# Performance work log

Hardware: AMD Instinct MI355X
Metric: run time of the kernel (lower is better)

## Reference

```python
import jax, jax.numpy as jnp
import numpy as np

N = 50000          # nodes
E = 1_600_000      # edges (avg degree 32)
F_IN = 512         # input feature dim
H = 256            # hidden_channels
C = 121            # num_classes (PPI)
L = 4              # num_layers
ALPHA = 0.5
THETA = 1.0


def setup_inputs() -> dict:
    key = jax.random.key(0)
    ks = jax.random.split(key, 8)
    x = jax.random.normal(ks[0], (N, F_IN), jnp.float32)
    edge_src = jax.random.randint(ks[1], (E,), 0, N, jnp.int32)
    edge_dst = jax.random.randint(ks[2], (E,), 0, N, jnp.int32)
    edge_weight = jax.random.uniform(ks[3], (E,), jnp.float32)
    s0 = 1.0 / np.sqrt(F_IN).astype(np.float32)
    lin0_w = jax.random.uniform(ks[4], (F_IN, H), jnp.float32, -s0, s0)
    lin0_b = jnp.zeros((H,), jnp.float32)
    conv_ws = jax.random.normal(ks[5], (L, H, H), jnp.float32) / np.float32(np.sqrt(H))
    s1 = 1.0 / np.sqrt(H).astype(np.float32)
    lin1_w = jax.random.uniform(ks[6], (H, C), jnp.float32, -s1, s1)
    lin1_b = jnp.zeros((C,), jnp.float32)
    return {
        "x": x, "edge_src": edge_src, "edge_dst": edge_dst,
        "edge_weight": edge_weight, "lin0_w": lin0_w, "lin0_b": lin0_b,
        "conv_ws": conv_ws, "lin1_w": lin1_w, "lin1_b": lin1_b,
    }


def reference(x, edge_src, edge_dst, edge_weight, lin0_w, lin0_b, conv_ws, lin1_w, lin1_b):
    # input projection + relu (dropout p=0 -> identity)
    x = jax.nn.relu(x @ lin0_w + lin0_b)          # [N, H]
    x0 = x
    for layer in range(L):
        beta = np.float32(np.log(THETA / (layer + 1) + 1.0))
        # sparse propagation: h = A @ x  (edge-wise gather * weight, scatter-add)
        msg = x[edge_src] * edge_weight[:, None]   # [E, H]
        h = jax.ops.segment_sum(msg, edge_dst, num_segments=N)  # [N, H]
        # GCN2Conv (shared_weights=True, normalize=False)
        h = (1.0 - ALPHA) * h + ALPHA * x0
        h = (1.0 - beta) * h + beta * (h @ conv_ws[layer])
        # residual + relu
        x = jax.nn.relu(h + x)
    return x @ lin1_w + lin1_b                    # [N, C]
```

## Files before the change

### kernel.cpp

```cpp
#include <hip/hip_runtime.h>
#include <math.h>

#define N_NODES 50000
#define E_EDGES 1600000
#define F_INDIM 512
#define H_DIM   256
#define C_OUT   121
#define L_LAYERS 4

typedef unsigned short u16;
typedef short bf16x8 __attribute__((ext_vector_type(8)));
typedef float f32x4  __attribute__((ext_vector_type(4)));

__device__ __forceinline__ float bf2f(u16 h) {
    return __uint_as_float(((unsigned int)h) << 16);
}
__device__ __forceinline__ u16 f2bf(float f) {
    unsigned int u = __float_as_uint(f);
    unsigned int r = u + 0x7FFFu + ((u >> 16) & 1u);
    return (u16)(r >> 16);
}

__global__ void prep_kernel(const float* __restrict__ l0w, const float* __restrict__ cw,
                            const float* __restrict__ l1w, u16* __restrict__ WT0,
                            u16* __restrict__ WTc, u16* __restrict__ WT1,
                            int* __restrict__ cnt) {
    int i = blockIdx.x * blockDim.x + threadIdx.x;
    if (i < 131072) {
        int n = i >> 9, k = i & 511;
        WT0[i] = f2bf(l0w[(long)k * H_DIM + n]);
        return;
    }
    i -= 131072;
    if (i < 262144) {
        int l = i >> 16, j = i & 65535, n = j >> 8, k = j & 255;
        WTc[(l << 16) + j] = f2bf(cw[(long)l * 65536 + (long)k * H_DIM + n]);
        return;
    }
    i -= 262144;
    if (i < 32768) {
        int n = i >> 8, k = i & 255;
        WT1[i] = (n < C_OUT) ? f2bf(l1w[(long)k * C_OUT + n]) : (u16)0;
        return;
    }
    i -= 32768;
    if (i < N_NODES) cnt[i] = 0;
}

__global__ void hist_kernel(const int* __restrict__ dst, int* __restrict__ deg) {
    int i = blockIdx.x * blockDim.x + threadIdx.x;
    if (i < E_EDGES / 4) {
        int4 d4 = reinterpret_cast<const int4*>(dst)[i];
        if (d4.x >= 0 && d4.x < N_NODES) atomicAdd(&deg[d4.x], 1);
        if (d4.y >= 0 && d4.y < N_NODES) atomicAdd(&deg[d4.y], 1);
        if (d4.z >= 0 && d4.z < N_NODES) atomicAdd(&deg[d4.z], 1);
        if (d4.w >= 0 && d4.w < N_NODES) atomicAdd(&deg[d4.w], 1);
    }
}

__global__ void scan_kernel(int* cnt, int* __restrict__ row_ptr) {
    __shared__ int sums[1024];
    const int t = threadIdx.x;
    const int CH = (N_NODES + 1023) / 1024;
    const int base = t * CH;
    int s = 0;
    for (int i = 0; i < CH; ++i) {
        int idx = base + i;
        if (idx < N_NODES) s += cnt[idx];
    }
    sums[t] = s;
    __syncthreads();
    for (int off = 1; off < 1024; off <<= 1) {
        int v = (t >= off) ? sums[t - off] : 0;
        __syncthreads();
        sums[t] += v;
        __syncthreads();
    }
    int run = (t == 0) ? 0 : sums[t - 1];
    for (int i = 0; i < CH; ++i) {
        int idx = base + i;
        if (idx < N_NODES) {
            int dv = cnt[idx];
            row_ptr[idx] = run;
            cnt[idx] = run;
            run += dv;
        }
    }
    if (t == 1023) row_ptr[N_NODES] = run;
}

__global__ void scatter_kernel(const int* __restrict__ src, const int* __restrict__ dst,
                               const float* __restrict__ w,
                               int* __restrict__ cnt, int* __restrict__ s_src,
                               float* __restrict__ s_w) {
    int i = blockIdx.x * blockDim.x + threadIdx.x;
    if (i < E_EDGES / 4) {
        int4   s4 = reinterpret_cast<const int4*>(src)[i];
        int4   d4 = reinterpret_cast<const int4*>(dst)[i];
        float4 w4 = reinterpret_cast<const float4*>(w)[i];
        int   sv[4] = {s4.x, s4.y, s4.z, s4.w};
        int   dv[4] = {d4.x, d4.y, d4.z, d4.w};
        float wv[4] = {w4.x, w4.y, w4.z, w4.w};
        #pragma unroll
        for (int u = 0; u < 4; ++u) {
            int d = dv[u];
            if (d < 0) d = 0; if (d >= N_NODES) d = N_NODES - 1;
            long idx = atomicAdd(&cnt[d], 1);
            if (idx < 0) idx = 0; if (idx >= E_EDGES) idx = E_EDGES - 1;
            s_src[idx] = sv[u];
            s_w[idx]   = wv[u];
        }
    }
}

template <int LAST>
__global__ __launch_bounds__(512) void layer_kernel(
        const int* __restrict__ row_ptr, const int* __restrict__ s_src,
        const float* __restrict__ s_w, const u16* __restrict__ Xin,
        const u16* __restrict__ X0, u16* __restrict__ Xout,
        const u16* __restrict__ WT, float beta,
        const u16* __restrict__ WT1, const float* __restrict__ l1b,
        float* __restrict__ outp) {
    __shared__ __align__(16) u16 hs[16 * H_DIM];
    const int w  = threadIdx.x >> 6;
    const int l  = threadIdx.x & 63;
    const int hi = l >> 4, lo = l & 15;
    const int half = l >> 5;
    const int q    = l & 31;
    const int bm = blockIdx.x * 16;

    for (int i = 0; i < 2; ++i) {
        const int rl  = w * 2 + i;
        const int row = bm + rl;
        int beg = row_ptr[row], end = row_ptr[row + 1];
        if (beg < 0) beg = 0; if (end > E_EDGES) end = E_EDGES;
        float accA[8] = {}, accB[8] = {};
        for (int e = beg; e < end; e += 4) {
            const int eA = e + half;
            const int eB = e + 2 + half;
            const int cA = (eA < end) ? eA : end - 1;
            const int cB = (eB < end) ? eB : end - 1;
            float wA = (eA < end) ? s_w[cA] : 0.f;
            float wB = (eB < end) ? s_w[cB] : 0.f;
            int sA = s_src[cA]; if (sA < 0) sA = 0; if (sA >= N_NODES) sA = N_NODES - 1;
            int sB = s_src[cB]; if (sB < 0) sB = 0; if (sB >= N_NODES) sB = N_NODES - 1;
            bf16x8 vA = *reinterpret_cast<const bf16x8*>(Xin + (long)sA * H_DIM + q * 8);
            bf16x8 vB = *reinterpret_cast<const bf16x8*>(Xin + (long)sB * H_DIM + q * 8);
            #pragma unroll
            for (int j = 0; j < 8; ++j) {
                accA[j] += wA * bf2f((u16)vA[j]);
                accB[j] += wB * bf2f((u16)vB[j]);
            }
        }
        float acc[8];
        #pragma unroll
        for (int j = 0; j < 8; ++j) {
            float s = accA[j] + accB[j];
            s += __shfl_xor(s, 32);
            acc[j] = s;
        }
        if (l < 32) {
            bf16x8 x0 = *reinterpret_cast<const bf16x8*>(X0 + (long)row * H_DIM + q * 8);
            bf16x8 ov;
            #pragma unroll
            for (int j = 0; j < 8; ++j)
                ov[j] = (short)f2bf(0.5f * acc[j] + 0.5f * bf2f((u16)x0[j]));
            const int off = rl * 512 + ((q * 16) ^ ((rl & 7) << 4));
            *reinterpret_cast<bf16x8*>((char*)hs + off) = ov;
        }
    }
    __syncthreads();

    const int col0 = w * 32;
    f32x4 acc[2];
    acc[0] = (f32x4){0.f, 0.f, 0.f, 0.f};
    acc[1] = (f32x4){0.f, 0.f, 0.f, 0.f};

    for (int k0 = 0; k0 < H_DIM; k0 += 32) {
        const int aoff = lo * 512 + (((k0 * 2) + hi * 16) ^ ((lo & 7) << 4));
        bf16x8 a = *reinterpret_cast<const bf16x8*>((const char*)hs + aoff);
        #pragma unroll
        for (int t = 0; t < 2; ++t) {
            bf16x8 b = *reinterpret_cast<const bf16x8*>(
                    WT + (long)(col0 + t * 16 + lo) * H_DIM + k0 + hi * 8);
            acc[t] = __builtin_amdgcn_mfma_f32_16x16x32_bf16(a, b, acc[t], 0, 0, 0);
        }
    }

    if (LAST) __syncthreads();

    #pragma unroll
    for (int t = 0; t < 2; ++t) {
        const int col = col0 + t * 16 + lo;
        #pragma unroll
        for (int r = 0; r < 4; ++r) {
            const int rl  = hi * 4 + r;
            const int row = bm + rl;
            const int hoff = rl * 512 + ((col * 2) ^ ((rl & 7) << 4));
            float hv = bf2f(*reinterpret_cast<const u16*>((const char*)hs + hoff));
            long idx = (long)row * H_DIM + col;
            float v = (1.f - beta) * hv + beta * acc[t][r] + bf2f(Xin[idx]);
            u16 vb = f2bf(fmaxf(v, 0.f));
            if (!LAST) {
                Xout[idx] = vb;
            } else {
                *reinterpret_cast<u16*>((char*)hs + hoff) = vb;
            }
        }
    }

    if (LAST) {
        __syncthreads();
        const int c1 = w * 16;
        f32x4 acc2 = (f32x4){0.f, 0.f, 0.f, 0.f};
        for (int k0 = 0; k0 < H_DIM; k0 += 32) {
            const int aoff = lo * 512 + (((k0 * 2) + hi * 16) ^ ((lo & 7) << 4));
            bf16x8 a = *reinterpret_cast<const bf16x8*>((const char*)hs + aoff);
            bf16x8 b = *reinterpret_cast<const bf16x8*>(
                    WT1 + (long)(c1 + lo) * H_DIM + k0 + hi * 8);
            acc2 = __builtin_amdgcn_mfma_f32_16x16x32_bf16(a, b, acc2, 0, 0, 0);
        }
        const int col = c1 + lo;
        if (col < C_OUT) {
            const float bias = l1b[col];
            #pragma unroll
            for (int r = 0; r < 4; ++r) {
                const int row = bm + hi * 4 + r;
                outp[(long)row * C_OUT + col] = acc2[r] + bias;
            }
        }
    }
}

template <int K, int NT>
__global__ __launch_bounds__(256) void mfma_gemm_kernel(
        const float* __restrict__ Aptr, const u16* __restrict__ WT,
        const float* __restrict__ bias,
        u16* __restrict__ X, u16* __restrict__ X0) {
    const int w  = threadIdx.x >> 6;
    const int l  = threadIdx.x & 63;
    const int hi = l >> 4, lo = l & 15;
    const int bm = blockIdx.x * 16;
    const int col0 = w * (NT * 16);

    f32x4 acc[NT];
    #pragma unroll
    for (int t = 0; t < NT; ++t) acc[t] = (f32x4){0.f, 0.f, 0.f, 0.f};

    for (int k0 = 0; k0 < K; k0 += 32) {
        bf16x8 a;
        const float* ap = Aptr + (long)(bm + lo) * K + k0 + hi * 8;
        float4 f0 = *reinterpret_cast<const float4*>(ap);
        float4 f1 = *reinterpret_cast<const float4*>(ap + 4);
        a[0] = (short)f2bf(f0.x); a[1] = (short)f2bf(f0.y);
        a[2] = (short)f2bf(f0.z); a[3] = (short)f2bf(f0.w);
        a[4] = (short)f2bf(f1.x); a[5] = (short)f2bf(f1.y);
        a[6] = (short)f2bf(f1.z); a[7] = (short)f2bf(f1.w);
        #pragma unroll
        for (int t = 0; t < NT; ++t) {
            bf16x8 b = *reinterpret_cast<const bf16x8*>(
                    WT + (long)(col0 + t * 16 + lo) * K + k0 + hi * 8);
            acc[t] = __builtin_amdgcn_mfma_f32_16x16x32_bf16(a, b, acc[t], 0, 0, 0);
        }
    }

    #pragma unroll
    for (int t = 0; t < NT; ++t) {
        const int col = col0 + t * 16 + lo;
        #pragma unroll
        for (int r = 0; r < 4; ++r) {
            const int row = bm + hi * 4 + r;
            float v = fmaxf(acc[t][r] + bias[col], 0.f);
            u16 h = f2bf(v);
            long idx = (long)row * H_DIM + col;
            X[idx] = h; X0[idx] = h;
        }
    }
}

extern "C" void kernel_launch(void* const* d_in, const int* in_sizes, int n_in,
                              void* d_out, int out_size, void* d_ws, size_t ws_size,
                              hipStream_t stream) {
    const float* x_in = (const float*)d_in[0];
    const int*   esrc = (const int*)d_in[1];
    const int*   edst = (const int*)d_in[2];
    const float* ew   = (const float*)d_in[3];
    const float* l0w  = (const float*)d_in[4];
    const float* l0b  = (const float*)d_in[5];
    const float* cw   = (const float*)d_in[6];
    const float* l1w  = (const float*)d_in[7];
    const float* l1b  = (const float*)d_in[8];
    float* out = (float*)d_out;
    (void)in_sizes; (void)n_in; (void)out_size;

    char* ws = (char*)d_ws;
    auto al = [](size_t x) { return (x + 255) & ~(size_t)255; };
    size_t o = 0;
    const size_t NHb = (size_t)N_NODES * H_DIM * sizeof(u16);
    u16* Xa = (u16*)(ws + o);  o += al(NHb);
    u16* Xb = (u16*)(ws + o);  o += al(NHb);
    u16* X0 = (u16*)(ws + o);  o += al(NHb);
    int* row_ptr = (int*)(ws + o); o += al((N_NODES + 1) * sizeof(int));
    int* cnt     = (int*)(ws + o); o += al((size_t)N_NODES * sizeof(int));
    int* s_src   = (int*)(ws + o); o += al((size_t)E_EDGES * sizeof(int));
    float* s_w   = (float*)(ws + o); o += al((size_t)E_EDGES * sizeof(float));
    u16* WT0 = (u16*)(ws + o); o += al((size_t)H_DIM * F_INDIM * sizeof(u16));
    u16* WTc = (u16*)(ws + o); o += al((size_t)L_LAYERS * H_DIM * H_DIM * sizeof(u16));
    u16* WT1 = (u16*)(ws + o); o += al((size_t)128 * H_DIM * sizeof(u16));
    if (ws_size < o) return;

    const int MBLK = N_NODES / 16;

    prep_kernel<<<1860, 256, 0, stream>>>(l0w, cw, l1w, WT0, WTc, WT1, cnt);

    mfma_gemm_kernel<F_INDIM, 4><<<MBLK, 256, 0, stream>>>(x_in, WT0, l0b, Xa, X0);

    hist_kernel<<<(E_EDGES / 4 + 255) / 256, 256, 0, stream>>>(edst, cnt);
    scan_kernel<<<1, 1024, 0, stream>>>(cnt, row_ptr);
    scatter_kernel<<<(E_EDGES / 4 + 255) / 256, 256, 0, stream>>>(esrc, edst, ew,
                                                                  cnt, s_src, s_w);

    u16* Xcur = Xa;
    u16* Xnxt = Xb;
    for (int l = 0; l < L_LAYERS - 1; ++l) {
        float beta = logf(1.0f / (float)(l + 1) + 1.0f);
        layer_kernel<0><<<MBLK, 512, 0, stream>>>(
            row_ptr, s_src, s_w, Xcur, X0, Xnxt,
            WTc + (size_t)l * H_DIM * H_DIM, beta,
            nullptr, nullptr, nullptr);
        u16* tmp = Xcur; Xcur = Xnxt; Xnxt = tmp;
    }
    {
        const int l = L_LAYERS - 1;
        float beta = logf(1.0f / (float)(l + 1) + 1.0f);
        layer_kernel<1><<<MBLK, 512, 0, stream>>>(
            row_ptr, s_src, s_w, Xcur, X0, nullptr,
            WTc + (size_t)l * H_DIM * H_DIM, beta,
            WT1, l1b, out);
    }
}
```

Baseline: 1.096 ms.

## Stage block edge lists in LDS and retile input projection GEMM

```diff
diff --git a/kernel.cpp b/kernel.cpp
--- a/kernel.cpp
+++ b/kernel.cpp
@@ -7,6 +7,7 @@
 #define H_DIM   256
 #define C_OUT   121
 #define L_LAYERS 4
+#define MCAP    1280
 
 typedef unsigned short u16;
 typedef short bf16x8 __attribute__((ext_vector_type(8)));
@@ -122,12 +123,25 @@
         const u16* __restrict__ WT1, const float* __restrict__ l1b,
         float* __restrict__ outp) {
     __shared__ __align__(16) u16 hs[16 * H_DIM];
+    __shared__ int   ms_src[MCAP];
+    __shared__ float ms_w[MCAP];
     const int w  = threadIdx.x >> 6;
     const int l  = threadIdx.x & 63;
     const int hi = l >> 4, lo = l & 15;
     const int half = l >> 5;
     const int q    = l & 31;
     const int bm = blockIdx.x * 16;
+
+    const int mbeg = row_ptr[bm];
+    int mspan = row_ptr[bm + 16] - mbeg;
+    if (mspan < 0) mspan = 0;
+    const int mlim = (mspan < MCAP) ? mspan : MCAP;
+    for (int j = threadIdx.x; j < mlim; j += 512) {
+        long gj = (long)mbeg + j;
+        if (gj >= 0 && gj < E_EDGES) { ms_src[j] = s_src[gj]; ms_w[j] = s_w[gj]; }
+        else                         { ms_src[j] = 0;         ms_w[j] = 0.f; }
+    }
+    __syncthreads();
 
     for (int i = 0; i < 2; ++i) {
         const int rl  = w * 2 + i;
@@ -140,10 +154,18 @@
             const int eB = e + 2 + half;
             const int cA = (eA < end) ? eA : end - 1;
             const int cB = (eB < end) ? eB : end - 1;
-            float wA = (eA < end) ? s_w[cA] : 0.f;
-            float wB = (eB < end) ? s_w[cB] : 0.f;
-            int sA = s_src[cA]; if (sA < 0) sA = 0; if (sA >= N_NODES) sA = N_NODES - 1;
-            int sB = s_src[cB]; if (sB < 0) sB = 0; if (sB >= N_NODES) sB = N_NODES - 1;
+            const int rA = cA - mbeg;
+            const int rB = cB - mbeg;
+            int sA; float wA;
+            int sB; float wB;
+            if (rA >= 0 && rA < MCAP) { sA = ms_src[rA]; wA = ms_w[rA]; }
+            else                      { sA = s_src[cA];  wA = s_w[cA]; }
+            if (rB >= 0 && rB < MCAP) { sB = ms_src[rB]; wB = ms_w[rB]; }
+            else                      { sB = s_src[cB];  wB = s_w[cB]; }
+            if (eA >= end) wA = 0.f;
+            if (eB >= end) wB = 0.f;
+            if (sA < 0) sA = 0; if (sA >= N_NODES) sA = N_NODES - 1;
+            if (sB < 0) sB = 0; if (sB >= N_NODES) sB = N_NODES - 1;
             bf16x8 vA = *reinterpret_cast<const bf16x8*>(Xin + (long)sA * H_DIM + q * 8);
             bf16x8 vB = *reinterpret_cast<const bf16x8*>(Xin + (long)sB * H_DIM + q * 8);
             #pragma unroll
@@ -232,50 +254,64 @@
     }
 }
 
-template <int K, int NT>
-__global__ __launch_bounds__(256) void mfma_gemm_kernel(
+__global__ __launch_bounds__(512) void lin0_kernel(
         const float* __restrict__ Aptr, const u16* __restrict__ WT,
         const float* __restrict__ bias,
         u16* __restrict__ X, u16* __restrict__ X0) {
     const int w  = threadIdx.x >> 6;
     const int l  = threadIdx.x & 63;
     const int hi = l >> 4, lo = l & 15;
-    const int bm = blockIdx.x * 16;
-    const int col0 = w * (NT * 16);
-
-    f32x4 acc[NT];
+    const int bm = blockIdx.x * 32;
+    const int col0 = w * 32;
+
+    f32x4 acc[2][2];
     #pragma unroll
-    for (int t = 0; t < NT; ++t) acc[t] = (f32x4){0.f, 0.f, 0.f, 0.f};
-
-    for (int k0 = 0; k0 < K; k0 += 32) {
-        bf16x8 a;
-        const float* ap = Aptr + (long)(bm + lo) * K + k0 + hi * 8;
-        float4 f0 = *reinterpret_cast<const float4*>(ap);
-        float4 f1 = *reinterpret_cast<const float4*>(ap + 4);
-        a[0] = (short)f2bf(f0.x); a[1] = (short)f2bf(f0.y);
-        a[2] = (short)f2bf(f0.z); a[3] = (short)f2bf(f0.w);
-        a[4] = (short)f2bf(f1.x); a[5] = (short)f2bf(f1.y);
-        a[6] = (short)f2bf(f1.z); a[7] = (short)f2bf(f1.w);
-        #pragma unroll
-        for (int t = 0; t < NT; ++t) {
+    for (int h = 0; h < 2; ++h)
+        #pragma unroll
+        for (int t = 0; t < 2; ++t) acc[h][t] = (f32x4){0.f, 0.f, 0.f, 0.f};
+
+    for (int k0 = 0; k0 < F_INDIM; k0 += 32) {
+        bf16x8 a[2];
+        #pragma unroll
+        for (int h = 0; h < 2; ++h) {
+            const int grow = bm + h * 16 + lo;
+            bf16x8 av = {0, 0, 0, 0, 0, 0, 0, 0};
+            if (grow < N_NODES) {
+                const float* ap = Aptr + (long)grow * F_INDIM + k0 + hi * 8;
+                float4 f0 = *reinterpret_cast<const float4*>(ap);
+                float4 f1 = *reinterpret_cast<const float4*>(ap + 4);
+                av[0] = (short)f2bf(f0.x); av[1] = (short)f2bf(f0.y);
+                av[2] = (short)f2bf(f0.z); av[3] = (short)f2bf(f0.w);
+                av[4] = (short)f2bf(f1.x); av[5] = (short)f2bf(f1.y);
+                av[6] = (short)f2bf(f1.z); av[7] = (short)f2bf(f1.w);
+            }
+            a[h] = av;
+        }
+        #pragma unroll
+        for (int t = 0; t < 2; ++t) {
             bf16x8 b = *reinterpret_cast<const bf16x8*>(
-                    WT + (long)(col0 + t * 16 + lo) * K + k0 + hi * 8);
-            acc[t] = __builtin_amdgcn_mfma_f32_16x16x32_bf16(a, b, acc[t], 0, 0, 0);
+                    WT + (long)(col0 + t * 16 + lo) * F_INDIM + k0 + hi * 8);
+            acc[0][t] = __builtin_amdgcn_mfma_f32_16x16x32_bf16(a[0], b, acc[0][t], 0, 0, 0);
+            acc[1][t] = __builtin_amdgcn_mfma_f32_16x16x32_bf16(a[1], b, acc[1][t], 0, 0, 0);
         }
     }
 
     #pragma unroll
-    for (int t = 0; t < NT; ++t) {
-        const int col = col0 + t * 16 + lo;
-        #pragma unroll
-        for (int r = 0; r < 4; ++r) {
-            const int row = bm + hi * 4 + r;
-            float v = fmaxf(acc[t][r] + bias[col], 0.f);
-            u16 h = f2bf(v);
-            long idx = (long)row * H_DIM + col;
-            X[idx] = h; X0[idx] = h;
-        }
-    }
+    for (int h = 0; h < 2; ++h)
+        #pragma unroll
+        for (int t = 0; t < 2; ++t) {
+            const int col = col0 + t * 16 + lo;
+            #pragma unroll
+            for (int r = 0; r < 4; ++r) {
+                const int row = bm + h * 16 + hi * 4 + r;
+                if (row < N_NODES) {
+                    float v = fmaxf(acc[h][t][r] + bias[col], 0.f);
+                    u16 hb = f2bf(v);
+                    long idx = (long)row * H_DIM + col;
+                    X[idx] = hb; X0[idx] = hb;
+                }
+            }
+        }
 }
 
 extern "C" void kernel_launch(void* const* d_in, const int* in_sizes, int n_in,
@@ -313,7 +349,7 @@
 
     prep_kernel<<<1860, 256, 0, stream>>>(l0w, cw, l1w, WT0, WTc, WT1, cnt);
 
-    mfma_gemm_kernel<F_INDIM, 4><<<MBLK, 256, 0, stream>>>(x_in, WT0, l0b, Xa, X0);
+    lin0_kernel<<<(N_NODES + 31) / 32, 512, 0, stream>>>(x_in, WT0, l0b, Xa, X0);
 
     hist_kernel<<<(E_EDGES / 4 + 255) / 256, 256, 0, stream>>>(edst, cnt);
     scan_kernel<<<1, 1024, 0, stream>>>(cnt, row_ptr);
```

Measured after the change: 1.065 ms. 2.9% less time.
